# Performance work log

Hardware: AMD Instinct MI355X
Metric: run time of the kernel (lower is better)

The kernel has to match this reference:

```python
import jax, jax.numpy as jnp
import numpy as np

B, T, DM, H, DQ, FF, L, OUT = 4, 512, 768, 8, 32, 3072, 6, 80
D_REL = 100   # relative_positional_distance
NEG = 1e8
LN_EPS = 1e-5


def _layer_norm(x, w, b):
    mu = jnp.mean(x, axis=-1, keepdims=True)
    var = jnp.mean((x - mu) ** 2, axis=-1, keepdims=True)
    return (x - mu) * jax.lax.rsqrt(var + LN_EPS) * w + b


def _attention(x, wq, wk, wv, wo, rel):
    # x: (B,T,DM); wq/wk/wv: (H,DM,DQ); wo: (H,DQ,DM); rel: (H, 2*D_REL-1, DQ)
    Tq = x.shape[1]
    q = jnp.einsum('btf,hfa->bhta', x, wq) / (DQ ** 0.5)   # q pre-scaled (as in source)
    k = jnp.einsum('btf,hfa->bhta', x, wk)
    v = jnp.einsum('btf,hfa->bhta', x, wv)
    logits = jnp.einsum('bhqa,bhka->bhqk', q, k)

    # relative positional logits over the 199 learned offsets
    rel_log = jnp.einsum('bhqd,hmd->bhqm', q, rel)          # (B,H,T,2*D_REL-1)
    pad = Tq - D_REL
    if pad > 0:
        # zero-pad to 2T-1 rel positions, then mask out-of-range offsets with -1e8
        rel_log = jnp.pad(rel_log, ((0, 0), (0, 0), (0, 0), (pad, pad)))
        m = jnp.arange(2 * Tq - 1)
        oob = (m < pad) | (m >= 2 * Tq - 1 - pad)
        rel_log = rel_log - NEG * oob.astype(rel_log.dtype)
    else:
        start = D_REL - Tq
        rel_log = rel_log[..., start:start + 2 * Tq - 1]
    # relative -> absolute indexing: pos[..., i, j] = rel_log[..., i, (j - i) + T - 1]
    idx = jnp.arange(Tq)[None, :] - jnp.arange(Tq)[:, None] + (Tq - 1)   # (T,T)
    pos = jnp.take_along_axis(rel_log, idx[None, None], axis=-1)         # (B,H,T,T)

    probs = jax.nn.softmax(logits + pos, axis=-1)
    o = jnp.einsum('bhqk,bhka->bhqa', probs, v)
    return jnp.einsum('bhta,had->btd', o, wo)


def _forward(x, wq, wk, wv, wo, rel, lin1_w, lin1_b, lin2_w, lin2_b,
             ln1_w, ln1_b, ln2_w, ln2_b, w_out, b_out):
    def step(h, p):
        (q, k, v, o, r, l1w, l1b, l2w, l2b, n1w, n1b, n2w, n2b) = p
        a = _attention(h, q, k, v, o, r)
        h = _layer_norm(h + a, n1w, n1b)                  # post-norm, residual
        ff = jnp.maximum(h @ l1w.T + l1b, 0.0) @ l2w.T + l2b
        h = _layer_norm(h + ff, n2w, n2b)
        return h, None
    h, _ = jax.lax.scan(step, x, (wq, wk, wv, wo, rel, lin1_w, lin1_b,
                                  lin2_w, lin2_b, ln1_w, ln1_b, ln2_w, ln2_b))
    return h @ w_out.T + b_out                            # (B,T,OUT)


def setup_inputs() -> dict:
    key = jax.random.key(0)
    ks = jax.random.split(key, 16)
    n = lambda k, shape, scale: (jax.random.normal(k, shape, dtype=jnp.float32) * scale)
    s_qkv = (2.0 / (DM + DQ)) ** 0.5      # xavier_normal_ scale
    s_o = (2.0 / (DQ + DM)) ** 0.5
    return {
        'x':      n(ks[0], (B, T, DM), 1.0),
        'wq':     n(ks[1], (L, H, DM, DQ), s_qkv),
        'wk':     n(ks[2], (L, H, DM, DQ), s_qkv),
        'wv':     n(ks[3], (L, H, DM, DQ), s_qkv),
        'wo':     n(ks[4], (L, H, DQ, DM), s_o),
        'rel':    n(ks[5], (L, H, 2 * D_REL - 1, DQ), DQ ** -0.5),
        'lin1_w': n(ks[6], (L, FF, DM), DM ** -0.5),
        'lin1_b': jnp.zeros((L, FF), jnp.float32),
        'lin2_w': n(ks[7], (L, DM, FF), FF ** -0.5),
        'lin2_b': jnp.zeros((L, DM), jnp.float32),
        'ln1_w':  jnp.ones((L, DM), jnp.float32),
        'ln1_b':  jnp.zeros((L, DM), jnp.float32),
        'ln2_w':  jnp.ones((L, DM), jnp.float32),
        'ln2_b':  jnp.zeros((L, DM), jnp.float32),
        'w_out':  n(ks[8], (OUT, DM), DM ** -0.5),
        'b_out':  jnp.zeros((OUT,), jnp.float32),
    }


def reference(x, wq, wk, wv, wo, rel, lin1_w, lin1_b, lin2_w, lin2_b,
              ln1_w, ln1_b, ln2_w, ln2_b, w_out, b_out):
    return _forward(x, wq, wk, wv, wo, rel, lin1_w, lin1_b, lin2_w, lin2_b,
                    ln1_w, ln1_b, ln2_w, ln2_b, w_out, b_out)
```

## Files before the change

### kernel.cpp

```cpp
#include <hip/hip_runtime.h>

typedef _Float16 f16;
typedef f16 f16x8 __attribute__((ext_vector_type(8)));
typedef f16 f16x4 __attribute__((ext_vector_type(4)));
typedef float f32x4 __attribute__((ext_vector_type(4)));

#define B_ 4
#define T_ 512
#define DM_ 768
#define H_ 8
#define DQ_ 32
#define FF_ 3072
#define L_ 6
#define OUT_ 80
#define M_ (B_*T_)

__device__ __forceinline__ void gload16(const f16* g, f16* l) {
    __builtin_amdgcn_global_load_lds(
        (const __attribute__((address_space(1))) unsigned int*)g,
        (__attribute__((address_space(3))) unsigned int*)l, 16, 0, 0);
}

template<int N> __device__ __forceinline__ void wait_vm() {
    if constexpr (N == 0)      asm volatile("s_waitcnt vmcnt(0)" ::: "memory");
    else if constexpr (N == 3) asm volatile("s_waitcnt vmcnt(3)" ::: "memory");
    else if constexpr (N == 4) asm volatile("s_waitcnt vmcnt(4)" ::: "memory");
    else                       asm volatile("s_waitcnt vmcnt(0)" ::: "memory");
}


#define PK_V0 393216L
#define PK_V1 (PK_V0 + 3538944L)
#define PK_V2 (PK_V1 + 3538944L)
#define PKB_VEC 29184
#define PKB_LIN 1632
#define PKB_QKV 1728
#define PKB_WO  1152
#define PKB_TOTAL (PKB_VEC + PKB_LIN + PKB_QKV + PKB_WO)

__global__ void pack_all_kernel(
    const float* __restrict__ x, const float* __restrict__ wq, const float* __restrict__ wk,
    const float* __restrict__ wv, const float* __restrict__ wo, const float* __restrict__ rel,
    const float* __restrict__ lin1w, const float* __restrict__ lin2w, const float* __restrict__ wout,
    f16* __restrict__ xH, f16* __restrict__ BTqkv, f16* __restrict__ BTwo,
    f16* __restrict__ lin1H, f16* __restrict__ lin2H, f16* __restrict__ woutH, f16* __restrict__ relH)
{
    __shared__ float tile[64 * 33];
    const int bid = blockIdx.x, tid = threadIdx.x;
    if (bid < PKB_VEC) {
        const long id = (long)bid * 256 + tid;
        const float* src; f16* dst; long off;
        if (id < PK_V0)      { src = x;     dst = xH;    off = id; }
        else if (id < PK_V1) { src = lin1w; dst = lin1H; off = id - PK_V0; }
        else                 { src = lin2w; dst = lin2H; off = id - PK_V1; }
        const float4 v = ((const float4*)src)[off];
        f16x4 o; o[0] = (f16)v.x; o[1] = (f16)v.y; o[2] = (f16)v.z; o[3] = (f16)v.w;
        ((f16x4*)dst)[off] = o;
    } else if (bid < PKB_VEC + PKB_LIN) {
        const long u = (long)(bid - PKB_VEC) * 256 + tid;
        if (u < 98304) {
            const int k = (int)(u % 768), n = (int)(u / 768);
            woutH[u] = (n < OUT_) ? (f16)wout[n * 768 + k] : (f16)0;
        } else {
            const long v2 = u - 98304;
            const int a = (int)(v2 & 31);
            const long t = v2 >> 5;
            const int d = (int)(t % 208);
            const int lh = (int)(t / 208);
            relH[v2] = (d < 199) ? (f16)rel[((long)lh * 199 + d) * 32 + a] : (f16)0;
        }
    } else if (bid < PKB_VEC + PKB_LIN + PKB_QKV) {
        const int g = bid - (PKB_VEC + PKB_LIN);
        const int kb = g % 12;
        const int grp = g / 12;
        const int h = grp & 7, sec = (grp >> 3) % 3, l = grp / 24;
        const float* w = (sec == 0) ? wq : (sec == 1 ? wk : wv);
        const float* src = w + (((long)l * 8 + h) * 768 + kb * 64) * 32;
        const float scale = (sec == 0) ? 0.17677669529663687f : 1.f;
#pragma unroll
        for (int p = 0; p < 8; ++p) {
            const int kk = p * 8 + (tid >> 5), a = tid & 31;
            tile[kk * 33 + a] = src[(long)kk * 32 + a] * scale;
        }
        __syncthreads();
        f16* dst = BTqkv + ((long)l * 768 + sec * 256 + h * 32) * 768 + kb * 64;
#pragma unroll
        for (int p = 0; p < 8; ++p) {
            const int a = p * 4 + (tid >> 6), kk = tid & 63;
            dst[(long)a * 768 + kk] = (f16)tile[kk * 33 + a];
        }
    } else {
        const int g = bid - (PKB_VEC + PKB_LIN + PKB_QKV);
        const int nb = g % 24;
        const int tmp = g / 24;
        const int kb2 = tmp % 8, l = tmp / 8;
        const float* src = wo + ((long)l * 256 + kb2 * 32) * 768 + nb * 32;
#pragma unroll
        for (int p = 0; p < 4; ++p) {
            const int r = p * 8 + (tid >> 5), c = tid & 31;
            tile[r * 33 + c] = src[(long)r * 768 + c];
        }
        __syncthreads();
        f16* dst = BTwo + ((long)l * 768 + nb * 32) * 256 + kb2 * 32;
#pragma unroll
        for (int p = 0; p < 4; ++p) {
            const int rr = p * 8 + (tid >> 5), cc = tid & 31;
            dst[(long)rr * 256 + cc] = (f16)tile[cc * 33 + rr];
        }
    }
}

__device__ __forceinline__ void xcd_tile(int BM, int BN, int& m0, int& n0) {
    const int gx = gridDim.x;
    const int id = blockIdx.y * gx + blockIdx.x;
    const int cpx = (gx * gridDim.y) >> 3;
    const int t = (id & 7) * cpx + (id >> 3);
    m0 = (t / gx) * BM;
    n0 = (t % gx) * BN;
}


template<int BM, int BN>
__global__ __launch_bounds__(256) void gemm6_kernel(
    const f16* __restrict__ A, const f16* __restrict__ Bt,
    const float* __restrict__ bias, const float* __restrict__ res,
    float* __restrict__ outF, f16* __restrict__ outH, f16* __restrict__ vTout,
    int M, int N, int K, int mode, int ldOut, int nMax)
{
    constexpr int IA = BM / 32;
    constexpr int JF = BN / 32;
    constexpr int LA = BM / 32;
    constexpr int LB = BN / 32;
    constexpr int L  = LA + LB;
    __shared__ __align__(16) f16 As[3][BM * 64];
    __shared__ __align__(16) f16 Bs[3][BN * 64];
    const int tid = threadIdx.x;
    const int wave = tid >> 6, lane = tid & 63;
    int m0, n0; xcd_tile(BM, BN, m0, n0);
    const int z = blockIdx.z;
    const int Kl = K / (int)gridDim.z;
    const int kb = z * Kl;
    const int nt = Kl / 64;
    const int wr = wave >> 1, wc = wave & 1;
    const int l15 = lane & 15, l4 = lane >> 4;
    const int lrow = lane >> 3;
    const int lcol = ((lane & 7) ^ (lane >> 3)) * 8;

    const f16* Abase = A  + (long)(m0 + lrow) * K + kb + lcol;
    const f16* Bbase = Bt + (long)(n0 + lrow) * K + kb + lcol;

    f32x4 acc[IA][JF];
#pragma unroll
    for (int i = 0; i < IA; ++i)
#pragma unroll
        for (int j = 0; j < JF; ++j) acc[i][j] = (f32x4){0.f, 0.f, 0.f, 0.f};

    auto stage = [&](int buf, int k0) {
#pragma unroll
        for (int i = 0; i < LA; ++i) {
            const int c = wave + 4 * i;
            gload16(Abase + (long)c * 8 * K + k0, &As[buf][c * 512]);
        }
#pragma unroll
        for (int i = 0; i < LB; ++i) {
            const int c = wave + 4 * i;
            gload16(Bbase + (long)c * 8 * K + k0, &Bs[buf][c * 512]);
        }
    };

    stage(0, 0);
    stage(1, 64);
    int cur = 0;
    for (int t = 0; t < nt; ++t) {
        if (t + 1 < nt) wait_vm<L>(); else wait_vm<0>();
        __builtin_amdgcn_s_barrier();
        if (t + 2 < nt) stage((t + 2) % 3, (t + 2) * 64);
#pragma unroll
        for (int s = 0; s < 2; ++s) {
            f16x8 af[IA], bf[JF];
#pragma unroll
            for (int i = 0; i < IA; ++i) {
                const int row = wr * (BM / 2) + i * 16 + l15;
                af[i] = *(const f16x8*)&As[cur][row * 64 + (((s * 4 + l4) ^ (l15 & 7)) * 8)];
            }
#pragma unroll
            for (int j = 0; j < JF; ++j) {
                const int row = wc * (BN / 2) + j * 16 + l15;
                bf[j] = *(const f16x8*)&Bs[cur][row * 64 + (((s * 4 + l4) ^ (l15 & 7)) * 8)];
            }
#pragma unroll
            for (int i = 0; i < IA; ++i)
#pragma unroll
                for (int j = 0; j < JF; ++j)
                    acc[i][j] = __builtin_amdgcn_mfma_f32_16x16x32_f16(af[i], bf[j], acc[i][j], 0, 0, 0);
        }
        cur = (cur + 1) % 3;
    }

#pragma unroll
    for (int i = 0; i < IA; ++i) {
#pragma unroll
        for (int j = 0; j < JF; ++j) {
            const int col = n0 + wc * (BN / 2) + j * 16 + l15;
            if (mode & 32) {
#pragma unroll
                for (int r = 0; r < 4; ++r) {
                    const int row = m0 + wr * (BM / 2) + i * 16 + l4 * 4 + r;
                    float v = acc[i][j][r];
                    if (col < 512) {
                        outH[(long)row * 512 + col] = (f16)v;
                    } else {
                        const int bb = row >> 9, t = row & 511;
                        vTout[((long)(bb * 256 + (col - 512))) * 512 + t] = (f16)v;
                    }
                }
            } else if (mode & 64) {
                float* po = outF + (long)z * M * ldOut;
#pragma unroll
                for (int r = 0; r < 4; ++r) {
                    const int row = m0 + wr * (BM / 2) + i * 16 + l4 * 4 + r;
                    po[(long)row * ldOut + col] = acc[i][j][r];
                }
            } else if (col < nMax) {
                const float bvv = (mode & 1) ? bias[col] : 0.f;
#pragma unroll
                for (int r = 0; r < 4; ++r) {
                    const int row = m0 + wr * (BM / 2) + i * 16 + l4 * 4 + r;
                    float v = acc[i][j][r] + bvv;
                    if (mode & 2) v += res[(long)row * N + col];
                    if (mode & 4) v = fmaxf(v, 0.f);
                    if (mode & 8)  outF[(long)row * ldOut + col] = v;
                    if (mode & 16) outH[(long)row * ldOut + col] = (f16)v;
                }
            }
        }
    }
}


__global__ __launch_bounds__(256) void attn_kernel(
    const f16* __restrict__ qkvH, const f16* __restrict__ vT,
    const f16* __restrict__ relH, int l, f16* __restrict__ o)
{
    __shared__ __align__(16) f16 Qs[64 * 40];
    __shared__ __align__(16) f16 Ks[288 * 40];
    __shared__ __align__(16) f16 Vt[32 * 296];
    __shared__ __align__(16) f16 Ps[64 * 296];
    __shared__ __align__(16) f16 Rl[64 * 216];
    const int tid = threadIdx.x;
    const int qb = blockIdx.x, h = blockIdx.y, b = blockIdx.z;
    const int q0 = qb * 64;
    int lo = q0 - 99; lo = (lo > 0) ? (lo & ~7) : 0;
    const int hi = min(512, q0 + 163);
    const int nk = hi - lo;

    {
        const int r = tid >> 2, c = tid & 3;
        *(f16x8*)&Qs[r * 40 + c * 8] =
            *(const f16x8*)(qkvH + ((long)(b * 512 + q0 + r)) * 512 + h * 32 + c * 8);
    }
    for (int idx = tid; idx < 288 * 4; idx += 256) {
        const int r = idx >> 2, c = idx & 3;
        f16x8 v = {};
        if (r < nk)
            v = *(const f16x8*)(qkvH + ((long)(b * 512 + lo + r)) * 512 + 256 + h * 32 + c * 8);
        *(f16x8*)&Ks[r * 40 + c * 8] = v;
    }
    for (int idx = tid; idx < 32 * 36; idx += 256) {
        const int a = idx / 36, k8 = idx % 36;
        f16x8 v = {};
        const int kbase = k8 * 8;
        if (kbase < nk) {
            const f16* src = vT + ((long)(b * 256 + h * 32 + a)) * 512 + lo + kbase;
            if (kbase + 8 <= nk) {
                v = *(const f16x8*)src;
            } else {
#pragma unroll
                for (int e = 0; e < 8; ++e) if (kbase + e < nk) v[e] = src[e];
            }
        }
        *(f16x8*)&Vt[a * 296 + kbase] = v;
    }
    __syncthreads();

    const int wave = tid >> 6, lane = tid & 63;
    const int l15 = lane & 15, l4 = lane >> 4;
    const int qloc = wave * 16;

    const f16x8 qf = *(const f16x8*)&Qs[(qloc + l15) * 40 + l4 * 8];

    const f16* relh = relH + ((long)(l * 8 + h)) * 208 * 32;
    {
        f32x4 racc[13];
#pragma unroll
        for (int fd = 0; fd < 13; ++fd) {
            const f16x8 bf = *(const f16x8*)(relh + (fd * 16 + l15) * 32 + l4 * 8);
            racc[fd] = __builtin_amdgcn_mfma_f32_16x16x32_f16(qf, bf, (f32x4){0.f,0.f,0.f,0.f}, 0, 0, 0);
        }
#pragma unroll
        for (int fd = 0; fd < 13; ++fd)
#pragma unroll
            for (int r = 0; r < 4; ++r)
                Rl[(qloc + l4 * 4 + r) * 216 + fd * 16 + l15] = (f16)racc[fd][r];
    }

    f32x4 sacc[18];
#pragma unroll
    for (int fk = 0; fk < 18; ++fk) {
        const f16x8 bf = *(const f16x8*)&Ks[(fk * 16 + l15) * 40 + l4 * 8];
        sacc[fk] = __builtin_amdgcn_mfma_f32_16x16x32_f16(qf, bf, (f32x4){0.f,0.f,0.f,0.f}, 0, 0, 0);
    }

    float mx[4] = {-1e30f, -1e30f, -1e30f, -1e30f};
#pragma unroll
    for (int fk = 0; fk < 18; ++fk) {
        const int kk = fk * 16 + l15;
        const int k = lo + kk;
#pragma unroll
        for (int r = 0; r < 4; ++r) {
            const int q = q0 + qloc + l4 * 4 + r;
            const int d = k - q + 99;
            float v = -1e30f;
            if (kk < nk && d >= 0 && d < 199)
                v = sacc[fk][r] + (float)Rl[(qloc + l4 * 4 + r) * 216 + d];
            sacc[fk][r] = v;
            mx[r] = fmaxf(mx[r], v);
        }
    }
#pragma unroll
    for (int r = 0; r < 4; ++r) {
        mx[r] = fmaxf(mx[r], __shfl_xor(mx[r], 1));
        mx[r] = fmaxf(mx[r], __shfl_xor(mx[r], 2));
        mx[r] = fmaxf(mx[r], __shfl_xor(mx[r], 4));
        mx[r] = fmaxf(mx[r], __shfl_xor(mx[r], 8));
    }
    float sum[4] = {0.f, 0.f, 0.f, 0.f};
#pragma unroll
    for (int fk = 0; fk < 18; ++fk) {
        const int kk = fk * 16 + l15;
#pragma unroll
        for (int r = 0; r < 4; ++r) {
            const float p = __expf(sacc[fk][r] - mx[r]);
            sum[r] += p;
            Ps[(qloc + l4 * 4 + r) * 296 + kk] = (f16)p;
        }
    }
#pragma unroll
    for (int r = 0; r < 4; ++r) {
        sum[r] += __shfl_xor(sum[r], 1);
        sum[r] += __shfl_xor(sum[r], 2);
        sum[r] += __shfl_xor(sum[r], 4);
        sum[r] += __shfl_xor(sum[r], 8);
    }

    f32x4 oacc[2] = {{0.f,0.f,0.f,0.f}, {0.f,0.f,0.f,0.f}};
#pragma unroll
    for (int ks = 0; ks < 9; ++ks) {
        const f16x8 pa = *(const f16x8*)&Ps[(qloc + l15) * 296 + ks * 32 + l4 * 8];
#pragma unroll
        for (int j = 0; j < 2; ++j) {
            const f16x8 vb = *(const f16x8*)&Vt[(j * 16 + l15) * 296 + ks * 32 + l4 * 8];
            oacc[j] = __builtin_amdgcn_mfma_f32_16x16x32_f16(pa, vb, oacc[j], 0, 0, 0);
        }
    }

    f16* ob = o + ((long)(b * 512 + q0 + qloc + l4 * 4)) * 256 + h * 32;
#pragma unroll
    for (int r = 0; r < 4; ++r) {
        const float inv = 1.f / sum[r];
#pragma unroll
        for (int j = 0; j < 2; ++j)
            ob[(long)r * 256 + j * 16 + l15] = (f16)(oacc[j][r] * inv);
    }
}


__global__ __launch_bounds__(256) void ln_kernel(
    const float* __restrict__ src, const float* __restrict__ w, const float* __restrict__ bb,
    float* __restrict__ outF, f16* __restrict__ outH)
{
    __shared__ float red1[4], red2[4];
    const int row = blockIdx.x, tid = threadIdx.x;
    const float* x = src + (long)row * 768;
    float v0 = x[tid], v1 = x[tid + 256], v2 = x[tid + 512];
    float s = v0 + v1 + v2;
#pragma unroll
    for (int off = 32; off > 0; off >>= 1) s += __shfl_xor(s, off);
    if ((tid & 63) == 0) red1[tid >> 6] = s;
    __syncthreads();
    const float mu = (red1[0] + red1[1] + red1[2] + red1[3]) * (1.f / 768.f);
    const float d0 = v0 - mu, d1 = v1 - mu, d2 = v2 - mu;
    float ss = d0 * d0 + d1 * d1 + d2 * d2;
#pragma unroll
    for (int off = 32; off > 0; off >>= 1) ss += __shfl_xor(ss, off);
    if ((tid & 63) == 0) red2[tid >> 6] = ss;
    __syncthreads();
    const float var = (red2[0] + red2[1] + red2[2] + red2[3]) * (1.f / 768.f);
    const float inv = rsqrtf(var + 1e-5f);
    float y0 = d0 * inv * w[tid]       + bb[tid];
    float y1 = d1 * inv * w[tid + 256] + bb[tid + 256];
    float y2 = d2 * inv * w[tid + 512] + bb[tid + 512];
    long base = (long)row * 768;
    outF[base + tid] = y0; outF[base + tid + 256] = y1; outF[base + tid + 512] = y2;
    outH[base + tid] = (f16)y0; outH[base + tid + 256] = (f16)y1; outH[base + tid + 512] = (f16)y2;
}


__global__ __launch_bounds__(256) void ln_sum2_kernel(
    const float* __restrict__ p,
    const float* __restrict__ bias, const float* __restrict__ res,
    const float* __restrict__ w, const float* __restrict__ bb,
    float* __restrict__ outF, f16* __restrict__ outH)
{
    __shared__ float red1[4], red2[4];
    const int row = blockIdx.x, tid = threadIdx.x;
    const long rb = (long)row * 768;
    float v[3];
#pragma unroll
    for (int i = 0; i < 3; ++i) {
        const int c = tid + i * 256;
        v[i] = bias[c] + res[rb + c] + p[rb + c] + p[(long)M_ * 768 + rb + c];
    }
    float s = v[0] + v[1] + v[2];
#pragma unroll
    for (int off = 32; off > 0; off >>= 1) s += __shfl_xor(s, off);
    if ((tid & 63) == 0) red1[tid >> 6] = s;
    __syncthreads();
    const float mu = (red1[0] + red1[1] + red1[2] + red1[3]) * (1.f / 768.f);
    const float d0 = v[0] - mu, d1 = v[1] - mu, d2 = v[2] - mu;
    float ss = d0 * d0 + d1 * d1 + d2 * d2;
#pragma unroll
    for (int off = 32; off > 0; off >>= 1) ss += __shfl_xor(ss, off);
    if ((tid & 63) == 0) red2[tid >> 6] = ss;
    __syncthreads();
    const float var = (red2[0] + red2[1] + red2[2] + red2[3]) * (1.f / 768.f);
    const float inv = rsqrtf(var + 1e-5f);
    float y0 = d0 * inv * w[tid]       + bb[tid];
    float y1 = d1 * inv * w[tid + 256] + bb[tid + 256];
    float y2 = d2 * inv * w[tid + 512] + bb[tid + 512];
    outF[rb + tid] = y0; outF[rb + tid + 256] = y1; outF[rb + tid + 512] = y2;
    outH[rb + tid] = (f16)y0; outH[rb + tid + 256] = (f16)y1; outH[rb + tid + 512] = (f16)y2;
}


extern "C" void kernel_launch(void* const* d_in, const int* in_sizes, int n_in,
                              void* d_out, int out_size, void* d_ws, size_t ws_size,
                              hipStream_t stream) {
    const float* x     = (const float*)d_in[0];
    const float* wq    = (const float*)d_in[1];
    const float* wk    = (const float*)d_in[2];
    const float* wv    = (const float*)d_in[3];
    const float* wo    = (const float*)d_in[4];
    const float* rel   = (const float*)d_in[5];
    const float* lin1w = (const float*)d_in[6];
    const float* lin1b = (const float*)d_in[7];
    const float* lin2w = (const float*)d_in[8];
    const float* lin2b = (const float*)d_in[9];
    const float* ln1w  = (const float*)d_in[10];
    const float* ln1b  = (const float*)d_in[11];
    const float* ln2w  = (const float*)d_in[12];
    const float* ln2b  = (const float*)d_in[13];
    const float* wout  = (const float*)d_in[14];
    const float* bout  = (const float*)d_in[15];

    char* base = (char*)d_ws;
    size_t off = 0;
    auto alloc = [&](size_t bytes) {
        void* p = base + off;
        off = (off + bytes + 255) & ~(size_t)255;
        return p;
    };
    f16*   xH    = (f16*)  alloc((size_t)M_ * 768 * 2);
    f16*   BTqkv = (f16*)  alloc((size_t)L_ * 768 * 768 * 2);
    f16*   BTwo  = (f16*)  alloc((size_t)L_ * 768 * 256 * 2);
    f16*   lin1H = (f16*)  alloc((size_t)L_ * 3072 * 768 * 2);
    f16*   lin2H = (f16*)  alloc((size_t)L_ * 768 * 3072 * 2);
    f16*   woutH = (f16*)  alloc((size_t)128 * 768 * 2);
    f16*   relH  = (f16*)  alloc((size_t)L_ * 8 * 208 * 32 * 2);
    f16*   qkvH  = (f16*)  alloc((size_t)M_ * 512 * 2);
    f16*   vTbuf = (f16*)  alloc((size_t)B_ * 256 * 512 * 2);
    float* scrF  = (float*)alloc((size_t)M_ * 768 * 4);
    float* part  = (float*)alloc((size_t)2 * M_ * 768 * 4);
    f16*   oH    = (f16*)  alloc((size_t)M_ * 256 * 2);
    float* ln1F  = (float*)alloc((size_t)M_ * 768 * 4);
    f16*   ln1H  = (f16*)  alloc((size_t)M_ * 768 * 2);
    f16*   ffH   = (f16*)  alloc((size_t)M_ * 3072 * 2);
    float* hF    = (float*)alloc((size_t)M_ * 768 * 4);
    f16*   hH    = (f16*)  alloc((size_t)M_ * 768 * 2);
    (void)ws_size; (void)in_sizes; (void)n_in; (void)out_size;

    pack_all_kernel<<<PKB_TOTAL, 256, 0, stream>>>(
        x, wq, wk, wv, wo, rel, lin1w, lin2w, wout,
        xH, BTqkv, BTwo, lin1H, lin2H, woutH, relH);

    for (int l = 0; l < L_; ++l) {
        const f16*   aIn   = (l == 0) ? xH : hH;
        const float* resIn = (l == 0) ? x  : hF;
        gemm6_kernel<32, 64><<<dim3(12, 64, 1), 256, 0, stream>>>(
            aIn, BTqkv + (size_t)l * 768 * 768, nullptr, nullptr, nullptr, qkvH, vTbuf,
            M_, 768, 768, 32, 512, 768);
        attn_kernel<<<dim3(8, 8, 4), 256, 0, stream>>>(qkvH, vTbuf, relH, l, oH);
        gemm6_kernel<32, 64><<<dim3(12, 64, 1), 256, 0, stream>>>(
            oH, BTwo + (size_t)l * 768 * 256, nullptr, resIn, scrF, nullptr, nullptr,
            M_, 768, 256, 2 | 8, 768, 768);
        ln_kernel<<<M_, 256, 0, stream>>>(scrF, ln1w + l * 768, ln1b + l * 768, ln1F, ln1H);
        gemm6_kernel<64, 64><<<dim3(48, 32, 1), 256, 0, stream>>>(
            ln1H, lin1H + (size_t)l * 3072 * 768, lin1b + l * 3072, nullptr, nullptr, ffH, nullptr,
            M_, 3072, 768, 1 | 4 | 16, 3072, 3072);
        gemm6_kernel<64, 64><<<dim3(12, 32, 2), 256, 0, stream>>>(
            ffH, lin2H + (size_t)l * 768 * 3072, nullptr, nullptr, part, nullptr, nullptr,
            M_, 768, 3072, 64, 768, 768);
        ln_sum2_kernel<<<M_, 256, 0, stream>>>(part, lin2b + l * 768, ln1F,
                                               ln2w + l * 768, ln2b + l * 768, hF, hH);
    }
    gemm6_kernel<32, 64><<<dim3(2, 64, 1), 256, 0, stream>>>(
        hH, woutH, bout, nullptr, (float*)d_out, nullptr, nullptr,
        M_, 80, 768, 1 | 8, 80, 80);
}
```

Measured before the change: 566.1 us.

## Vectorize weight packing, double-buffer GEMM, enlarge FFN tiles and split-K to four

The pack kernel now moves eight fp16 values per thread and uses float4 loads with 16-byte stores for the transposes, so it issues fewer memory operations. The GEMM drops from a triple-buffered LDS pipeline with a two-stage prefetch to a double buffer that prefetches one stage and adds a second barrier per k-step. The FFN GEMMs move to 128x64 tiles, and lin2 uses a 4-way split-K, so the second layer norm now sums four partial buffers. This cuts the pack kernel's instruction count and changes occupancy and reuse in the GEMMs, but prefetch depth drops, every k-step pays an extra barrier, and the larger split-K partials add memory traffic.

Measured after the change: 512.7 us. -9.4%, faster.

```diff
diff --git a/kernel.cpp b/kernel.cpp
--- a/kernel.cpp
+++ b/kernel.cpp
@@ -25,14 +25,16 @@
     if constexpr (N == 0)      asm volatile("s_waitcnt vmcnt(0)" ::: "memory");
     else if constexpr (N == 3) asm volatile("s_waitcnt vmcnt(3)" ::: "memory");
     else if constexpr (N == 4) asm volatile("s_waitcnt vmcnt(4)" ::: "memory");
+    else if constexpr (N == 6) asm volatile("s_waitcnt vmcnt(6)" ::: "memory");
+    else if constexpr (N == 8) asm volatile("s_waitcnt vmcnt(8)" ::: "memory");
     else                       asm volatile("s_waitcnt vmcnt(0)" ::: "memory");
 }
 
 
-#define PK_V0 393216L
-#define PK_V1 (PK_V0 + 3538944L)
-#define PK_V2 (PK_V1 + 3538944L)
-#define PKB_VEC 29184
+#define PKU_X  196608L
+#define PKU_L1 (PKU_X + 1769472L)
+#define PKU_L2 (PKU_L1 + 1769472L)
+#define PKB_VEC 14592
 #define PKB_LIN 1632
 #define PKB_QKV 1728
 #define PKB_WO  1152
@@ -48,14 +50,17 @@
     __shared__ float tile[64 * 33];
     const int bid = blockIdx.x, tid = threadIdx.x;
     if (bid < PKB_VEC) {
-        const long id = (long)bid * 256 + tid;
+        const long u = (long)bid * 256 + tid;
         const float* src; f16* dst; long off;
-        if (id < PK_V0)      { src = x;     dst = xH;    off = id; }
-        else if (id < PK_V1) { src = lin1w; dst = lin1H; off = id - PK_V0; }
-        else                 { src = lin2w; dst = lin2H; off = id - PK_V1; }
-        const float4 v = ((const float4*)src)[off];
-        f16x4 o; o[0] = (f16)v.x; o[1] = (f16)v.y; o[2] = (f16)v.z; o[3] = (f16)v.w;
-        ((f16x4*)dst)[off] = o;
+        if (u < PKU_X)       { src = x;     dst = xH;    off = u; }
+        else if (u < PKU_L1) { src = lin1w; dst = lin1H; off = u - PKU_X; }
+        else                 { src = lin2w; dst = lin2H; off = u - PKU_L1; }
+        const float4 v0 = ((const float4*)src)[off * 2];
+        const float4 v1 = ((const float4*)src)[off * 2 + 1];
+        f16x8 o;
+        o[0] = (f16)v0.x; o[1] = (f16)v0.y; o[2] = (f16)v0.z; o[3] = (f16)v0.w;
+        o[4] = (f16)v1.x; o[5] = (f16)v1.y; o[6] = (f16)v1.z; o[7] = (f16)v1.w;
+        ((f16x8*)dst)[off] = o;
     } else if (bid < PKB_VEC + PKB_LIN) {
         const long u = (long)(bid - PKB_VEC) * 256 + tid;
         if (u < 98304) {
@@ -78,16 +83,22 @@
         const float* src = w + (((long)l * 8 + h) * 768 + kb * 64) * 32;
         const float scale = (sec == 0) ? 0.17677669529663687f : 1.f;
 #pragma unroll
-        for (int p = 0; p < 8; ++p) {
-            const int kk = p * 8 + (tid >> 5), a = tid & 31;
-            tile[kk * 33 + a] = src[(long)kk * 32 + a] * scale;
+        for (int p = 0; p < 2; ++p) {
+            const int kk = p * 32 + (tid >> 3), a = (tid & 7) * 4;
+            const float4 v = *(const float4*)(src + (long)kk * 32 + a);
+            tile[kk * 33 + a]     = v.x * scale;
+            tile[kk * 33 + a + 1] = v.y * scale;
+            tile[kk * 33 + a + 2] = v.z * scale;
+            tile[kk * 33 + a + 3] = v.w * scale;
         }
         __syncthreads();
         f16* dst = BTqkv + ((long)l * 768 + sec * 256 + h * 32) * 768 + kb * 64;
-#pragma unroll
-        for (int p = 0; p < 8; ++p) {
-            const int a = p * 4 + (tid >> 6), kk = tid & 63;
-            dst[(long)a * 768 + kk] = (f16)tile[kk * 33 + a];
+        {
+            const int a = tid >> 3, k8 = (tid & 7) * 8;
+            f16x8 o;
+#pragma unroll
+            for (int e = 0; e < 8; ++e) o[e] = (f16)tile[(k8 + e) * 33 + a];
+            *(f16x8*)(dst + (long)a * 768 + k8) = o;
         }
     } else {
         const int g = bid - (PKB_VEC + PKB_LIN + PKB_QKV);
@@ -95,17 +106,22 @@
         const int tmp = g / 24;
         const int kb2 = tmp % 8, l = tmp / 8;
         const float* src = wo + ((long)l * 256 + kb2 * 32) * 768 + nb * 32;
-#pragma unroll
-        for (int p = 0; p < 4; ++p) {
-            const int r = p * 8 + (tid >> 5), c = tid & 31;
-            tile[r * 33 + c] = src[(long)r * 768 + c];
+        {
+            const int r = tid >> 3, c = (tid & 7) * 4;
+            const float4 v = *(const float4*)(src + (long)r * 768 + c);
+            tile[r * 33 + c]     = v.x;
+            tile[r * 33 + c + 1] = v.y;
+            tile[r * 33 + c + 2] = v.z;
+            tile[r * 33 + c + 3] = v.w;
         }
         __syncthreads();
-        f16* dst = BTwo + ((long)l * 768 + nb * 32) * 256 + kb2 * 32;
-#pragma unroll
-        for (int p = 0; p < 4; ++p) {
-            const int rr = p * 8 + (tid >> 5), cc = tid & 31;
-            dst[(long)rr * 256 + cc] = (f16)tile[cc * 33 + rr];
+        if (tid < 128) {
+            const int n = tid >> 2, k8 = (tid & 3) * 8;
+            f16x8 o;
+#pragma unroll
+            for (int e = 0; e < 8; ++e) o[e] = (f16)tile[(k8 + e) * 33 + n];
+            f16* dst = BTwo + ((long)l * 768 + nb * 32 + n) * 256 + kb2 * 32 + k8;
+            *(f16x8*)dst = o;
         }
     }
 }
@@ -121,7 +137,7 @@
 
 
 template<int BM, int BN>
-__global__ __launch_bounds__(256) void gemm6_kernel(
+__global__ __launch_bounds__(256) void gemm7_kernel(
     const f16* __restrict__ A, const f16* __restrict__ Bt,
     const float* __restrict__ bias, const float* __restrict__ res,
     float* __restrict__ outF, f16* __restrict__ outH, f16* __restrict__ vTout,
@@ -132,8 +148,8 @@
     constexpr int LA = BM / 32;
     constexpr int LB = BN / 32;
     constexpr int L  = LA + LB;
-    __shared__ __align__(16) f16 As[3][BM * 64];
-    __shared__ __align__(16) f16 Bs[3][BN * 64];
+    __shared__ __align__(16) f16 As[2][BM * 64];
+    __shared__ __align__(16) f16 Bs[2][BN * 64];
     const int tid = threadIdx.x;
     const int wave = tid >> 6, lane = tid & 63;
     int m0, n0; xcd_tile(BM, BN, m0, n0);
@@ -169,12 +185,11 @@
     };
 
     stage(0, 0);
-    stage(1, 64);
     int cur = 0;
     for (int t = 0; t < nt; ++t) {
-        if (t + 1 < nt) wait_vm<L>(); else wait_vm<0>();
+        if (t + 1 < nt) { stage(cur ^ 1, (t + 1) * 64); wait_vm<L>(); }
+        else            { wait_vm<0>(); }
         __builtin_amdgcn_s_barrier();
-        if (t + 2 < nt) stage((t + 2) % 3, (t + 2) * 64);
 #pragma unroll
         for (int s = 0; s < 2; ++s) {
             f16x8 af[IA], bf[JF];
@@ -194,7 +209,8 @@
                 for (int j = 0; j < JF; ++j)
                     acc[i][j] = __builtin_amdgcn_mfma_f32_16x16x32_f16(af[i], bf[j], acc[i][j], 0, 0, 0);
         }
-        cur = (cur + 1) % 3;
+        __builtin_amdgcn_s_barrier();
+        cur ^= 1;
     }
 
 #pragma unroll
@@ -406,7 +422,7 @@
 }
 
 
-__global__ __launch_bounds__(256) void ln_sum2_kernel(
+__global__ __launch_bounds__(256) void ln_sum4_kernel(
     const float* __restrict__ p,
     const float* __restrict__ bias, const float* __restrict__ res,
     const float* __restrict__ w, const float* __restrict__ bb,
@@ -419,7 +435,10 @@
 #pragma unroll
     for (int i = 0; i < 3; ++i) {
         const int c = tid + i * 256;
-        v[i] = bias[c] + res[rb + c] + p[rb + c] + p[(long)M_ * 768 + rb + c];
+        float s = bias[c] + res[rb + c];
+#pragma unroll
+        for (int zz = 0; zz < 4; ++zz) s += p[((long)zz * M_ + row) * 768 + c];
+        v[i] = s;
     }
     float s = v[0] + v[1] + v[2];
 #pragma unroll
@@ -480,7 +499,7 @@
     f16*   qkvH  = (f16*)  alloc((size_t)M_ * 512 * 2);
     f16*   vTbuf = (f16*)  alloc((size_t)B_ * 256 * 512 * 2);
     float* scrF  = (float*)alloc((size_t)M_ * 768 * 4);
-    float* part  = (float*)alloc((size_t)2 * M_ * 768 * 4);
+    float* part  = (float*)alloc((size_t)4 * M_ * 768 * 4);
     f16*   oH    = (f16*)  alloc((size_t)M_ * 256 * 2);
     float* ln1F  = (float*)alloc((size_t)M_ * 768 * 4);
     f16*   ln1H  = (f16*)  alloc((size_t)M_ * 768 * 2);
@@ -496,24 +515,24 @@
     for (int l = 0; l < L_; ++l) {
         const f16*   aIn   = (l == 0) ? xH : hH;
         const float* resIn = (l == 0) ? x  : hF;
-        gemm6_kernel<32, 64><<<dim3(12, 64, 1), 256, 0, stream>>>(
+        gemm7_kernel<32, 64><<<dim3(12, 64, 1), 256, 0, stream>>>(
             aIn, BTqkv + (size_t)l * 768 * 768, nullptr, nullptr, nullptr, qkvH, vTbuf,
             M_, 768, 768, 32, 512, 768);
         attn_kernel<<<dim3(8, 8, 4), 256, 0, stream>>>(qkvH, vTbuf, relH, l, oH);
-        gemm6_kernel<32, 64><<<dim3(12, 64, 1), 256, 0, stream>>>(
+        gemm7_kernel<32, 64><<<dim3(12, 64, 1), 256, 0, stream>>>(
             oH, BTwo + (size_t)l * 768 * 256, nullptr, resIn, scrF, nullptr, nullptr,
             M_, 768, 256, 2 | 8, 768, 768);
         ln_kernel<<<M_, 256, 0, stream>>>(scrF, ln1w + l * 768, ln1b + l * 768, ln1F, ln1H);
-        gemm6_kernel<64, 64><<<dim3(48, 32, 1), 256, 0, stream>>>(
+        gemm7_kernel<128, 64><<<dim3(48, 16, 1), 256, 0, stream>>>(
             ln1H, lin1H + (size_t)l * 3072 * 768, lin1b + l * 3072, nullptr, nullptr, ffH, nullptr,
             M_, 3072, 768, 1 | 4 | 16, 3072, 3072);
-        gemm6_kernel<64, 64><<<dim3(12, 32, 2), 256, 0, stream>>>(
+        gemm7_kernel<128, 64><<<dim3(12, 16, 4), 256, 0, stream>>>(
             ffH, lin2H + (size_t)l * 768 * 3072, nullptr, nullptr, part, nullptr, nullptr,
             M_, 768, 3072, 64, 768, 768);
-        ln_sum2_kernel<<<M_, 256, 0, stream>>>(part, lin2b + l * 768, ln1F,
+        ln_sum4_kernel<<<M_, 256, 0, stream>>>(part, lin2b + l * 768, ln1F,
                                                ln2w + l * 768, ln2b + l * 768, hF, hH);
     }
-    gemm6_kernel<32, 64><<<dim3(2, 64, 1), 256, 0, stream>>>(
+    gemm7_kernel<32, 64><<<dim3(2, 64, 1), 256, 0, stream>>>(
         hH, woutH, bout, nullptr, (float*)d_out, nullptr, nullptr,
         M_, 80, 768, 1 | 8, 80, 80);
 }
```
